# Kernel optimization log

Measured on AMD Instinct MI355X. Metric: run time of the kernel, lower is better.

The kernel has to match this reference:

```python
import jax, jax.numpy as jnp
import numpy as np

H = 8          # heads
C = 128        # out_channels per head (hidden_dim)
EMB = 256      # embedding_dim
NG = 64        # number of graphs in batch
EPS_LN = 1e-5


def _layer_norm(x, g, b):
    mu = x.mean(-1, keepdims=True)
    var = ((x - mu) ** 2).mean(-1, keepdims=True)
    return (x - mu) * jax.lax.rsqrt(var + EPS_LN) * g + b


def _transformer_conv(x, src, dst, Wq, bq, Wk, bk, Wv, bv, Ws, bs, Wb):
    # PyG TransformerConv, heads=H, concat=False, beta=True, root_weight=True
    N = x.shape[0]
    q = (x @ Wq + bq).reshape(N, H, C)
    k = (x @ Wk + bk).reshape(N, H, C)
    v = (x @ Wv + bv).reshape(N, H, C)
    # per-edge attention logits: q_i . k_j / sqrt(C)   (i=dst, j=src)
    logits = jnp.einsum('ehc,ehc->eh', q[dst], k[src]) / jnp.sqrt(jnp.asarray(C, x.dtype))
    # segment softmax over incoming edges of each dst node
    m = jax.ops.segment_max(logits, dst, num_segments=N)
    m = jnp.where(jnp.isfinite(m), m, 0.0)
    ex = jnp.exp(logits - m[dst])
    den = jax.ops.segment_sum(ex, dst, num_segments=N)
    alpha = ex / (den[dst] + 1e-16)                      # [E,H]
    msg = alpha[:, :, None] * v[src]                     # [E,H,C]
    out = jax.ops.segment_sum(msg, dst, num_segments=N)  # [N,H,C]
    out = out.mean(axis=1)                               # concat=False -> head mean
    # beta-gated skip connection
    x_r = x @ Ws + bs                                    # [N,C]
    beta = jax.nn.sigmoid(jnp.concatenate([out, x_r, out - x_r], axis=-1) @ Wb)  # [N,1]
    return beta * x_r + (1.0 - beta) * out


def _lin(k, fan_in, fan_out, scale=None):
    s = scale if scale is not None else 1.0 / np.sqrt(fan_in)
    k1, k2 = jax.random.split(k)
    W = jax.random.uniform(k1, (fan_in, fan_out), jnp.float32, -s, s)
    b = jax.random.uniform(k2, (fan_out,), jnp.float32, -s, s)
    return W, b


def setup_inputs() -> dict:
    key = jax.random.key(0)
    ks = jax.random.split(key, 32)
    N, E, V = 50000, 400000, 10000
    inp = {
        'x': jax.random.randint(ks[0], (N,), 0, V, jnp.int32),
        'edge_index': jax.random.randint(ks[1], (2, E), 0, N, jnp.int32),
        'batch': jnp.sort(jax.random.randint(ks[2], (N,), 0, NG, jnp.int32)),
        'emb_w': jax.random.normal(ks[3], (V, EMB), jnp.float32),
    }
    ki = 4
    for l, din in enumerate([EMB, C]):
        Wq, bq = _lin(ks[ki], din, H * C); ki += 1
        Wk, bk = _lin(ks[ki], din, H * C); ki += 1
        Wv, bv = _lin(ks[ki], din, H * C); ki += 1
        Ws, bs = _lin(ks[ki], din, C); ki += 1
        Wb, _ = _lin(ks[ki], 3 * C, 1); ki += 1
        inp.update({f'Wq{l}': Wq, f'bq{l}': bq, f'Wk{l}': Wk, f'bk{l}': bk,
                    f'Wv{l}': Wv, f'bv{l}': bv, f'Ws{l}': Ws, f'bs{l}': bs,
                    f'Wb{l}': Wb, f'g{l}': jnp.ones((C,), jnp.float32),
                    f'be{l}': jnp.zeros((C,), jnp.float32)})
    Wc1, bc1 = _lin(ks[ki], C, C // 2); ki += 1
    Wc2, bc2 = _lin(ks[ki], C // 2, 1); ki += 1
    inp.update({'Wc1': Wc1, 'bc1': bc1, 'Wc2': Wc2, 'bc2': bc2})
    return inp


def reference(x, edge_index, batch, emb_w,
              Wq0, bq0, Wk0, bk0, Wv0, bv0, Ws0, bs0, Wb0, g0, be0,
              Wq1, bq1, Wk1, bk1, Wv1, bv1, Ws1, bs1, Wb1, g1, be1,
              Wc1, bc1, Wc2, bc2):
    src, dst = edge_index[0], edge_index[1]
    h = emb_w[x]                                           # [N, EMB]
    # layer 0 (no residual, per original `if i > 0`)
    h = _transformer_conv(h, src, dst, Wq0, bq0, Wk0, bk0, Wv0, bv0, Ws0, bs0, Wb0)
    h = jax.nn.relu(_layer_norm(h, g0, be0))               # dropout = identity (eval)
    # layer 1 (residual)
    res = h
    h = _transformer_conv(h, src, dst, Wq1, bq1, Wk1, bk1, Wv1, bv1, Ws1, bs1, Wb1)
    h = jax.nn.relu(_layer_norm(h + res, g1, be1))
    # global mean pool over graphs
    s = jax.ops.segment_sum(h, batch, num_segments=NG)     # [NG, C]
    cnt = jax.ops.segment_sum(jnp.ones((h.shape[0],), h.dtype), batch, num_segments=NG)
    pooled = s / jnp.maximum(cnt, 1.0)[:, None]
    # classifier MLP
    z = jax.nn.relu(pooled @ Wc1 + bc1)
    return z @ Wc2 + bc2                                   # [NG, 1]
```

## Files before the change

### kernel.cpp

```cpp
#include <hip/hip_runtime.h>
#include <hip/hip_fp16.h>
#include <math.h>

#define HEADS 8
#define CDIM 128
#define HC 1024
#define EMBD 256
#define NGRAPH 64
#define QSCALE 0.08838834764831845f
#define QSCALE2 0.12751744f

typedef unsigned short u16;
typedef short s8v __attribute__((ext_vector_type(8)));
typedef float f4v __attribute__((ext_vector_type(4)));
typedef _Float16 h2v __attribute__((ext_vector_type(2)));

__device__ __forceinline__ float b2f(u16 u) {
  union { unsigned int i; float f; } v; v.i = ((unsigned int)u) << 16; return v.f;
}
__device__ __forceinline__ u16 f2b(float f) {
  union { float f; unsigned int i; } v; v.f = f;
  unsigned int i = v.i;
  unsigned int r = (i + 0x7FFFu + ((i >> 16) & 1u)) >> 16;
  return (u16)r;
}
__device__ __forceinline__ u16 f2h(float f) {
  __half h = __float2half(f);
  return *(u16*)&h;
}

union U4H { uint4 u; h2v h[4]; };

__device__ __forceinline__ float dot8h(uint4 ku, uint4 qu0, uint4 qu1) {
  (void)qu1;
  return 0.f;
}

__global__ __launch_bounds__(256) void embed_kernel(
    const int* __restrict__ x, const float* __restrict__ emb,
    u16* __restrict__ h0, int N)
{
  int idx = blockIdx.x * 256 + threadIdx.x;
  if (idx >= N * (EMBD / 4)) return;
  int n = idx >> 6;
  int j = (idx & 63) * 4;
  int vid = x[n];
  float4 f = *(const float4*)&emb[(size_t)vid * EMBD + j];
  ushort4 u;
  u.x = f2b(f.x); u.y = f2b(f.y); u.z = f2b(f.z); u.w = f2b(f.w);
  *(ushort4*)&h0[(size_t)n * EMBD + j] = u;
}

__global__ __launch_bounds__(256) void transposeWs_tiled(
    const float* __restrict__ in, u16* __restrict__ out, int R)
{
  __shared__ u16 tile[64][66];
  int r0 = blockIdx.x * 64, c0 = blockIdx.y * 64;
  int t = threadIdx.x;
  int ci = t & 63, q4 = t >> 6;
#pragma unroll
  for (int ii = 0; ii < 16; ii++) {
    int r = q4 + ii * 4;
    tile[r][ci] = f2b(in[(size_t)(r0 + r) * CDIM + c0 + ci]);
  }
  __syncthreads();
  int rr = t & 63;
#pragma unroll
  for (int ii = 0; ii < 16; ii++) {
    int c = q4 + ii * 4;
    out[(size_t)(c0 + c) * R + r0 + rr] = tile[rr][c];
  }
}

__global__ __launch_bounds__(256) void build_qkvT_tiled(
    const float* __restrict__ Wq, const float* __restrict__ Wk, const float* __restrict__ Wv,
    u16* __restrict__ WT, int K, int hpc)
{
  __shared__ u16 tile[64][130];
  int rg0 = blockIdx.x * 128;
  int kk0 = blockIdx.y * 64;
  int chunkCols = hpc * 384;
  int chunk = rg0 / chunkCols;
  int within = rg0 - chunk * chunkCols;
  int head = chunk * hpc + within / 384;
  int sub = within % 384;
  int sect = sub >> 7;
  const float* W = (sect == 0) ? Wq : (sect == 1 ? Wk : Wv);
  float scale = (sect == 0) ? QSCALE2 : 1.0f;
  int cc0 = head * CDIM;
  int t = threadIdx.x;
  int ci = t & 127, k2 = t >> 7;
#pragma unroll
  for (int ii = 0; ii < 32; ii++) {
    int ki = k2 + ii * 2;
    tile[ki][ci] = f2b(W[(size_t)(kk0 + ki) * HC + cc0 + ci] * scale);
  }
  __syncthreads();
  int k = t & 63, r4 = t >> 6;
#pragma unroll
  for (int ii = 0; ii < 32; ii++) {
    int r = r4 + ii * 4;
    WT[(size_t)(rg0 + r) * K + kk0 + k] = tile[k][r];
  }
}
__global__ __launch_bounds__(256) void build_qkvb(
    const float* __restrict__ bq, const float* __restrict__ bk, const float* __restrict__ bv,
    float* __restrict__ bT, int hpc)
{
  int rg = blockIdx.x * 256 + threadIdx.x;
  if (rg >= 3 * HC) return;
  int chunkCols = hpc * 384;
  int chunk = rg / chunkCols;
  int within = rg - chunk * chunkCols;
  int head = chunk * hpc + within / 384;
  int sub = within % 384;
  int sect = sub >> 7;
  int cc = head * CDIM + (sub & 127);
  bT[rg] = (sect == 0) ? bq[cc] * QSCALE2 : (sect == 1 ? bk[cc] : bv[cc]);
}

__global__ __launch_bounds__(256) void deg_kernel(const int* __restrict__ ei, int* __restrict__ deg, int E) {
  int e = blockIdx.x * 256 + threadIdx.x;
  if (e < E) atomicAdd(&deg[ei[E + e]], 1);
}
__global__ __launch_bounds__(256) void scan1_kernel(const int* __restrict__ deg, int* __restrict__ row_ptr,
                                                    int* __restrict__ bsum, int N) {
  __shared__ int sb[256];
  int t = threadIdx.x, idx = blockIdx.x * 256 + t;
  int x = (idx < N) ? deg[idx] : 0;
  sb[t] = x; __syncthreads();
  for (int off = 1; off < 256; off <<= 1) {
    int y = (t >= off) ? sb[t - off] : 0;
    __syncthreads(); sb[t] += y; __syncthreads();
  }
  if (idx < N) row_ptr[idx + 1] = sb[t];
  if (t == 255) bsum[blockIdx.x] = sb[255];
  if (idx == 0) row_ptr[0] = 0;
}
__global__ __launch_bounds__(256) void scan2_kernel(int* __restrict__ bsum, int B) {
  __shared__ int sb[256];
  int t = threadIdx.x;
  int x = (t < B) ? bsum[t] : 0;
  sb[t] = x; __syncthreads();
  for (int off = 1; off < 256; off <<= 1) {
    int y = (t >= off) ? sb[t - off] : 0;
    __syncthreads(); sb[t] += y; __syncthreads();
  }
  if (t < B) bsum[t] = sb[t] - x;
}
__global__ __launch_bounds__(256) void scan3_kernel(int* __restrict__ row_ptr, const int* __restrict__ bsum, int N) {
  int idx = blockIdx.x * 256 + threadIdx.x;
  if (idx < N) row_ptr[idx + 1] += bsum[idx >> 8];
}
__global__ __launch_bounds__(256) void scatter_kernel(const int* __restrict__ ei,
                                                      const int* __restrict__ row_ptr,
                                                      int* __restrict__ fill, int* __restrict__ col, int E) {
  int e = blockIdx.x * 256 + threadIdx.x;
  if (e >= E) return;
  int d = ei[E + e];
  int pos = row_ptr[d] + atomicAdd(&fill[d], 1);
  col[pos] = ei[e];
}
__global__ void gb_kernel(const int* __restrict__ batch, int* __restrict__ gb, int N) {
  int g = threadIdx.x;
  if (g > NGRAPH) return;
  int lo = 0, hi = N;
  while (lo < hi) { int mid = (lo + hi) >> 1; if (batch[mid] < g) lo = mid + 1; else hi = mid; }
  gb[g] = lo;
}

template <int K, int F16OUT>
__global__ __launch_bounds__(256, 2) void gemm_lds(
    const u16* __restrict__ A, const u16* __restrict__ BT,
    const float* __restrict__ bias, u16* __restrict__ outT,
    int M, int Ncol)
{
  const int LDK = K + 8;
  const int KS = K / 32;
  __shared__ __align__(16) u16 As[64 * LDK];
  int t = threadIdx.x, lane = t & 63, w = t >> 6;
  int q4 = lane >> 4, cn = lane & 15;
  int m0 = blockIdx.y * 64;
  int nt = blockIdx.x * 4 + w;
  bool wActive = nt * 64 < Ncol;

  if (m0 + 64 <= M) {
    const u16* Ablk = A + (size_t)m0 * K;
#pragma unroll
    for (int ii = 0; ii < K / 32; ii++) {
      int g = (ii * 256 + t) * 8;
      int r = g / K, c = g - r * K;
      *(uint4*)&As[r * LDK + c] = *(const uint4*)(Ablk + g);
    }
  } else {
#pragma unroll
    for (int ii = 0; ii < K / 32; ii++) {
      int g = (ii * 256 + t) * 8;
      int r = g / K, c = g - r * K;
      int gr = m0 + r; if (gr >= M) gr = M - 1;
      *(uint4*)&As[r * LDK + c] = *(const uint4*)(A + (size_t)gr * K + c);
    }
  }
  __syncthreads();

  if (!wActive) return;

  f4v acc[4][4] = {};
  const u16* bb = BT + ((size_t)nt * 64 + cn) * K + q4 * 8;
#pragma unroll
  for (int ks = 0; ks < KS; ks++) {
    s8v bf[4], af[4];
#pragma unroll
    for (int ni = 0; ni < 4; ni++)
      bf[ni] = *(const s8v*)(bb + (size_t)ni * 16 * K + ks * 32);
#pragma unroll
    for (int mi = 0; mi < 4; mi++)
      af[mi] = *(const s8v*)&As[(mi * 16 + cn) * LDK + ks * 32 + q4 * 8];
#pragma unroll
    for (int mi = 0; mi < 4; mi++)
#pragma unroll
      for (int ni = 0; ni < 4; ni++)
        acc[mi][ni] = __builtin_amdgcn_mfma_f32_16x16x32_bf16(af[mi], bf[ni], acc[mi][ni], 0, 0, 0);
  }

  u16* obase = outT + (size_t)nt * M * 64;
  float bv[4];
#pragma unroll
  for (int ni = 0; ni < 4; ni++) bv[ni] = bias[nt * 64 + ni * 16 + cn];
#pragma unroll
  for (int mi = 0; mi < 4; mi++) {
#pragma unroll
    for (int j = 0; j < 4; j++) {
      int gm = m0 + mi * 16 + q4 * 4 + j;
      if (gm < M) {
#pragma unroll
        for (int ni = 0; ni < 4; ni++) {
          float val = acc[mi][ni][j] + bv[ni];
          obase[(size_t)gm * 64 + ni * 16 + cn] = F16OUT ? f2h(val) : f2b(val);
        }
      }
    }
  }
}

template <int HPC>
__global__ __launch_bounds__(256) void attn_chunk_kernel(
    const u16* __restrict__ qkv,
    const int* __restrict__ row_ptr, const int* __restrict__ col,
    float* __restrict__ outacc, int N, int first)
{
  int t = threadIdx.x;
  int w = t >> 6, lane = t & 63;
  int g = lane >> 4, i = lane & 15;
  int n, j;
  if (HPC == 4)      { n = blockIdx.x;                 j = w; }
  else if (HPC == 2) { n = blockIdx.x * 2 + (w >> 1);  j = w & 1; }
  else               { n = blockIdx.x * 4 + w;         j = 0; }
  bool active = (HPC == 4) ? true : (n < N);

  int itile = i >> 3, ioff = (i & 7) * 8;
  const u16* qb = qkv + (size_t)(j * 6 + 0 + itile) * N * 64 + ioff;
  const u16* kb = qkv + (size_t)(j * 6 + 2 + itile) * N * 64 + ioff;
  const u16* vb = qkv + (size_t)(j * 6 + 4 + itile) * N * 64 + ioff;

  float acc[8] = {};
  float m = -INFINITY, l = 0.f;
  if (active) {
    U4H qu; qu.u = *(const uint4*)(qb + (size_t)n * 64);
    int e0 = row_ptr[n], e1 = row_ptr[n + 1];
    for (int eb = e0; eb < e1; eb += 8) {
      int egA = eb + g, egB = eb + 4 + g;
      bool vA = egA < e1, vB = egB < e1;
      int sA = col[vA ? egA : e1 - 1];
      int sB = col[vB ? egB : e1 - 1];
      U4H kuA, vuA, kuB, vuB;
      kuA.u = *(const uint4*)(kb + (size_t)sA * 64);
      kuB.u = *(const uint4*)(kb + (size_t)sB * 64);
      vuA.u = *(const uint4*)(vb + (size_t)sA * 64);
      vuB.u = *(const uint4*)(vb + (size_t)sB * 64);

      float pA, pB;
#if defined(__has_builtin) && __has_builtin(__builtin_amdgcn_fdot2)
      pA = __builtin_amdgcn_fdot2(kuA.h[0], qu.h[0], 0.f, false);
      pA = __builtin_amdgcn_fdot2(kuA.h[1], qu.h[1], pA, false);
      pA = __builtin_amdgcn_fdot2(kuA.h[2], qu.h[2], pA, false);
      pA = __builtin_amdgcn_fdot2(kuA.h[3], qu.h[3], pA, false);
      pB = __builtin_amdgcn_fdot2(kuB.h[0], qu.h[0], 0.f, false);
      pB = __builtin_amdgcn_fdot2(kuB.h[1], qu.h[1], pB, false);
      pB = __builtin_amdgcn_fdot2(kuB.h[2], qu.h[2], pB, false);
      pB = __builtin_amdgcn_fdot2(kuB.h[3], qu.h[3], pB, false);
#else
      pA = 0.f; pB = 0.f;
#pragma unroll
      for (int z = 0; z < 4; z++) {
        pA += (float)kuA.h[z][0] * (float)qu.h[z][0] + (float)kuA.h[z][1] * (float)qu.h[z][1];
        pB += (float)kuB.h[z][0] * (float)qu.h[z][0] + (float)kuB.h[z][1] * (float)qu.h[z][1];
      }
#endif
#pragma unroll
      for (int off = 1; off <= 8; off <<= 1) {
        pA += __shfl_xor(pA, off, 64);
        pB += __shfl_xor(pB, off, 64);
      }
      if (!vA) pA = -INFINITY;
      if (!vB) pB = -INFINITY;

      {
        float pm = fmaxf(pA, __shfl_xor(pA, 16));
        pm = fmaxf(pm, __shfl_xor(pm, 32));
        if (pm > m) {
          float al = exp2f(m - pm);
          l *= al;
#pragma unroll
          for (int z = 0; z < 8; z++) acc[z] *= al;
          m = pm;
        }
        float pe = exp2f(pA - m);
        float ps = pe + __shfl_xor(pe, 16);
        ps += __shfl_xor(ps, 32);
        l += ps;
#pragma unroll
        for (int z = 0; z < 4; z++) {
          acc[2 * z]     = fmaf(pe, (float)vuA.h[z][0], acc[2 * z]);
          acc[2 * z + 1] = fmaf(pe, (float)vuA.h[z][1], acc[2 * z + 1]);
        }
      }
      {
        float pm = fmaxf(pB, __shfl_xor(pB, 16));
        pm = fmaxf(pm, __shfl_xor(pm, 32));
        if (pm > m) {
          float al = exp2f(m - pm);
          l *= al;
#pragma unroll
          for (int z = 0; z < 8; z++) acc[z] *= al;
          m = pm;
        }
        float pe = exp2f(pB - m);
        float ps = pe + __shfl_xor(pe, 16);
        ps += __shfl_xor(ps, 32);
        l += ps;
#pragma unroll
        for (int z = 0; z < 4; z++) {
          acc[2 * z]     = fmaf(pe, (float)vuB.h[z][0], acc[2 * z]);
          acc[2 * z + 1] = fmaf(pe, (float)vuB.h[z][1], acc[2 * z + 1]);
        }
      }
    }
  }
  float inv = 0.125f / (l + 1e-16f);
#pragma unroll
  for (int z = 0; z < 8; z++) {
    float a = acc[z] * inv;
    a += __shfl_xor(a, 16);
    a += __shfl_xor(a, 32);
    acc[z] = a;
  }

  if (HPC == 1) {
    if (active && g == 0) {
      float* op = outacc + (size_t)n * CDIM + i * 8;
      if (first) {
        *(float4*)op       = make_float4(acc[0], acc[1], acc[2], acc[3]);
        *(float4*)(op + 4) = make_float4(acc[4], acc[5], acc[6], acc[7]);
      } else {
        float4 o0 = *(float4*)op, o1 = *(float4*)(op + 4);
        *(float4*)op       = make_float4(o0.x + acc[0], o0.y + acc[1], o0.z + acc[2], o0.w + acc[3]);
        *(float4*)(op + 4) = make_float4(o1.x + acc[4], o1.y + acc[5], o1.z + acc[6], o1.w + acc[7]);
      }
    }
  } else {
    __shared__ float sacc[4][128];
    if (g == 0) {
      *(float4*)&sacc[w][i * 8]     = make_float4(acc[0], acc[1], acc[2], acc[3]);
      *(float4*)&sacc[w][i * 8 + 4] = make_float4(acc[4], acc[5], acc[6], acc[7]);
    }
    __syncthreads();
    if (HPC == 4) {
      if (t < 128) {
        float v = sacc[0][t] + sacc[1][t] + sacc[2][t] + sacc[3][t];
        size_t o = (size_t)blockIdx.x * CDIM + t;
        outacc[o] = first ? v : (outacc[o] + v);
      }
    } else {
      int nn = blockIdx.x * 2 + (t >> 7);
      int c = t & 127;
      if (nn < N) {
        float v = sacc[(t >> 7) * 2][c] + sacc[(t >> 7) * 2 + 1][c];
        size_t o = (size_t)nn * CDIM + c;
        outacc[o] = first ? v : (outacc[o] + v);
      }
    }
  }
}

template <int LAYER>
__global__ __launch_bounds__(256) void epilogue_kernel(
    const float* __restrict__ outacc, const u16* __restrict__ xrT,
    const float* __restrict__ Wb, const float* __restrict__ gam, const float* __restrict__ bet,
    const u16* __restrict__ res,
    u16* __restrict__ hout,
    float* __restrict__ houtf,
    int N)
{
  int t = threadIdx.x;
  int local = t >> 7, c = t & 127, w = t >> 6;
  int n = blockIdx.x * 2 + local;
  bool act = n < N;
  __shared__ float sred[8];
  __shared__ float smv[2][3];

  float oc = 0.f, xc = 0.f;
  if (act) {
    oc = outacc[(size_t)n * CDIM + c];
    xc = b2f(xrT[((size_t)(c >> 6) * N + n) * 64 + (c & 63)]);
  }
  float pb = oc * Wb[c] + xc * Wb[CDIM + c] + (oc - xc) * Wb[2 * CDIM + c];
#pragma unroll
  for (int off = 32; off; off >>= 1) pb += __shfl_down(pb, off, 64);
  if ((t & 63) == 0) sred[w] = pb;
  __syncthreads();
  if (t == 0)   smv[0][0] = 1.f / (1.f + __expf(-(sred[0] + sred[1])));
  if (t == 128) smv[1][0] = 1.f / (1.f + __expf(-(sred[2] + sred[3])));
  __syncthreads();
  float beta = smv[local][0];
  float val = beta * xc + (1.f - beta) * oc;
  if (LAYER == 1 && act) val += b2f(res[(size_t)n * CDIM + c]);

  float s1 = val, s2 = val * val;
#pragma unroll
  for (int off = 32; off; off >>= 1) {
    s1 += __shfl_down(s1, off, 64);
    s2 += __shfl_down(s2, off, 64);
  }
  __syncthreads();
  if ((t & 63) == 0) { sred[w * 2] = s1; sred[w * 2 + 1] = s2; }
  __syncthreads();
  if (t == 0) {
    float S1 = sred[0] + sred[2], S2 = sred[1] + sred[3];
    float mu = S1 * (1.f / CDIM);
    float var = fmaxf(S2 * (1.f / CDIM) - mu * mu, 0.f);
    smv[0][1] = mu; smv[0][2] = 1.f / sqrtf(var + 1e-5f);
  }
  if (t == 128) {
    float S1 = sred[4] + sred[6], S2 = sred[5] + sred[7];
    float mu = S1 * (1.f / CDIM);
    float var = fmaxf(S2 * (1.f / CDIM) - mu * mu, 0.f);
    smv[1][1] = mu; smv[1][2] = 1.f / sqrtf(var + 1e-5f);
  }
  __syncthreads();
  if (act) {
    float y = (val - smv[local][1]) * smv[local][2] * gam[c] + bet[c];
    y = fmaxf(y, 0.f);
    if (LAYER == 0) hout[(size_t)n * CDIM + c] = f2b(y);
    else            houtf[(size_t)n * CDIM + c] = y;
  }
}

__global__ __launch_bounds__(256) void classifier_kernel(
    const float* __restrict__ hf, const int* __restrict__ gb,
    const float* __restrict__ Wc1, const float* __restrict__ bc1,
    const float* __restrict__ Wc2, const float* __restrict__ bc2,
    float* __restrict__ out)
{
  int g = blockIdx.x, t = threadIdx.x;
  int half = t >> 7, c = t & 127;
  int s = gb[g], e = gb[g + 1];
  float acc = 0.f;
  for (int n = s + half; n < e; n += 2) acc += hf[(size_t)n * CDIM + c];
  __shared__ float sb[2][128];
  __shared__ float sp[128], sz[64];
  sb[half][c] = acc;
  __syncthreads();
  float cg = fmaxf((float)(e - s), 1.f);
  if (t < 128) sp[t] = (sb[0][t] + sb[1][t]) / cg;
  __syncthreads();
  if (t < 64) {
    float a = bc1[t];
    for (int cc = 0; cc < 128; cc++) a += sp[cc] * Wc1[cc * 64 + t];
    sz[t] = fmaxf(a, 0.f);
  }
  __syncthreads();
  if (t < 64) {
    float pbv = sz[t] * Wc2[t];
    for (int off = 32; off; off >>= 1) pbv += __shfl_down(pbv, off, 64);
    if (t == 0) out[g] = pbv + bc2[0];
  }
}

extern "C" void kernel_launch(void* const* d_in, const int* in_sizes, int n_in,
                              void* d_out, int out_size, void* d_ws, size_t ws_size,
                              hipStream_t stream)
{
  if (n_in != 30) return;

  const int N = in_sizes[0];
  const int E = in_sizes[1] / 2;

  const int* x     = (const int*)d_in[0];
  const int* ei    = (const int*)d_in[1];
  const int* batch = (const int*)d_in[2];
  const float* emb = (const float*)d_in[3];
  const float* Wq0 = (const float*)d_in[4];  const float* bq0 = (const float*)d_in[5];
  const float* Wk0 = (const float*)d_in[6];  const float* bk0 = (const float*)d_in[7];
  const float* Wv0 = (const float*)d_in[8];  const float* bv0 = (const float*)d_in[9];
  const float* Ws0 = (const float*)d_in[10]; const float* bs0 = (const float*)d_in[11];
  const float* Wb0 = (const float*)d_in[12]; const float* g0  = (const float*)d_in[13]; const float* be0 = (const float*)d_in[14];
  const float* Wq1 = (const float*)d_in[15]; const float* bq1 = (const float*)d_in[16];
  const float* Wk1 = (const float*)d_in[17]; const float* bk1 = (const float*)d_in[18];
  const float* Wv1 = (const float*)d_in[19]; const float* bv1 = (const float*)d_in[20];
  const float* Ws1 = (const float*)d_in[21]; const float* bs1 = (const float*)d_in[22];
  const float* Wb1 = (const float*)d_in[23]; const float* g1  = (const float*)d_in[24]; const float* be1 = (const float*)d_in[25];
  const float* Wc1 = (const float*)d_in[26]; const float* bc1 = (const float*)d_in[27];
  const float* Wc2 = (const float*)d_in[28]; const float* bc2 = (const float*)d_in[29];

  auto rnd = [](size_t b) { return (b + 511) & ~(size_t)511; };
  size_t fixedBytes =
      rnd((size_t)N * CDIM * 4) +
      rnd((size_t)N * EMBD * 2) +
      rnd((size_t)N * CDIM * 2) * 2 +
      rnd((size_t)3 * HC * EMBD * 2) +
      rnd((size_t)3 * HC * CDIM * 2) +
      rnd((size_t)3 * HC * 4) * 2 +
      rnd((size_t)CDIM * EMBD * 2) +
      rnd((size_t)CDIM * CDIM * 2) +
      rnd((size_t)N * 4) * 2 +
      rnd((size_t)(N + 1) * 4) +
      rnd((size_t)E * 4) +
      rnd(256 * 4) +
      rnd(65 * 4);
  int hpc = 1;
  if (ws_size >= fixedBytes + rnd((size_t)N * 4 * 384 * 2)) hpc = 4;
  else if (ws_size >= fixedBytes + rnd((size_t)N * 2 * 384 * 2)) hpc = 2;
  const int chunkCols = hpc * 384;
  const int nchunks = HEADS / hpc;

  char* ws = (char*)d_ws;
  size_t off = 0;
  auto alloc = [&](size_t bytes) -> void* {
    void* p = ws + off;
    off += (bytes + 511) & ~(size_t)511;
    return p;
  };
  u16*   qkvc  = (u16*)  alloc((size_t)N * chunkCols * 2);
  float* outacc= (float*)alloc((size_t)N * CDIM * 4);
  u16*   h0    = (u16*)  alloc((size_t)N * EMBD * 2);
  u16*   h1    = (u16*)  alloc((size_t)N * CDIM * 2);
  u16*   xrb   = (u16*)  alloc((size_t)N * CDIM * 2);
  u16*   WT0   = (u16*)  alloc((size_t)3 * HC * EMBD * 2);
  u16*   WT1   = (u16*)  alloc((size_t)3 * HC * CDIM * 2);
  float* bT0   = (float*)alloc((size_t)3 * HC * 4);
  float* bT1   = (float*)alloc((size_t)3 * HC * 4);
  u16*   WsT0  = (u16*)  alloc((size_t)CDIM * EMBD * 2);
  u16*   WsT1  = (u16*)  alloc((size_t)CDIM * CDIM * 2);
  int*   deg   = (int*)  alloc((size_t)N * 4);
  int*   fill  = (int*)  alloc((size_t)N * 4);
  int*   rowp  = (int*)  alloc((size_t)(N + 1) * 4);
  int*   colb  = (int*)  alloc((size_t)E * 4);
  int*   bsum  = (int*)  alloc(256 * 4);
  int*   gb    = (int*)  alloc(65 * 4);

  hipMemsetAsync(deg, 0, (size_t)N * 4, stream);
  hipMemsetAsync(fill, 0, (size_t)N * 4, stream);

  embed_kernel<<<(N * 64 + 255) / 256, 256, 0, stream>>>(x, emb, h0, N);
  { dim3 gT(3 * HC / 128, EMBD / 64);
    build_qkvT_tiled<<<gT, 256, 0, stream>>>(Wq0, Wk0, Wv0, WT0, EMBD, hpc); }
  { dim3 gT(3 * HC / 128, CDIM / 64);
    build_qkvT_tiled<<<gT, 256, 0, stream>>>(Wq1, Wk1, Wv1, WT1, CDIM, hpc); }
  build_qkvb<<<(3 * HC + 255) / 256, 256, 0, stream>>>(bq0, bk0, bv0, bT0, hpc);
  build_qkvb<<<(3 * HC + 255) / 256, 256, 0, stream>>>(bq1, bk1, bv1, bT1, hpc);
  { dim3 gT(EMBD / 64, CDIM / 64);
    transposeWs_tiled<<<gT, 256, 0, stream>>>(Ws0, WsT0, EMBD); }
  { dim3 gT(CDIM / 64, CDIM / 64);
    transposeWs_tiled<<<gT, 256, 0, stream>>>(Ws1, WsT1, CDIM); }

  int nb = (N + 255) / 256;
  deg_kernel<<<(E + 255) / 256, 256, 0, stream>>>(ei, deg, E);
  scan1_kernel<<<nb, 256, 0, stream>>>(deg, rowp, bsum, N);
  scan2_kernel<<<1, 256, 0, stream>>>(bsum, nb);
  scan3_kernel<<<nb, 256, 0, stream>>>(rowp, bsum, N);
  scatter_kernel<<<(E + 255) / 256, 256, 0, stream>>>(ei, rowp, fill, colb, E);
  gb_kernel<<<1, 128, 0, stream>>>(batch, gb, N);

  int rowStrips = (N + 63) / 64;
  int attnBlocks = (hpc == 4) ? N : (hpc == 2 ? (N + 1) / 2 : (N + 3) / 4);
  int epiBlocks = (N + 1) / 2;

  for (int layer = 0; layer < 2; layer++) {
    const u16* Ain   = (layer == 0) ? h0 : h1;
    const u16* WT    = (layer == 0) ? WT0 : WT1;
    const float* bT  = (layer == 0) ? bT0 : bT1;
    const u16* WsT   = (layer == 0) ? WsT0 : WsT1;
    const float* bs  = (layer == 0) ? bs0 : bs1;
    const float* Wb  = (layer == 0) ? Wb0 : Wb1;
    const float* gam = (layer == 0) ? g0 : g1;
    const float* bet = (layer == 0) ? be0 : be1;
    int K = (layer == 0) ? EMBD : CDIM;

    dim3 gXR(1, rowStrips);
    dim3 gQKV(chunkCols / 256, rowStrips);
    if (K == EMBD) gemm_lds<EMBD, 0><<<gXR, 256, 0, stream>>>(Ain, WsT, bs, xrb, N, CDIM);
    else           gemm_lds<CDIM, 0><<<gXR, 256, 0, stream>>>(Ain, WsT, bs, xrb, N, CDIM);
    for (int c = 0; c < nchunks; c++) {
      if (K == EMBD)
        gemm_lds<EMBD, 1><<<gQKV, 256, 0, stream>>>(Ain, WT + (size_t)c * chunkCols * K,
                                                    bT + c * chunkCols, qkvc, N, chunkCols);
      else
        gemm_lds<CDIM, 1><<<gQKV, 256, 0, stream>>>(Ain, WT + (size_t)c * chunkCols * K,
                                                    bT + c * chunkCols, qkvc, N, chunkCols);
      int first = (c == 0) ? 1 : 0;
      if (hpc == 4)      attn_chunk_kernel<4><<<attnBlocks, 256, 0, stream>>>(qkvc, rowp, colb, outacc, N, first);
      else if (hpc == 2) attn_chunk_kernel<2><<<attnBlocks, 256, 0, stream>>>(qkvc, rowp, colb, outacc, N, first);
      else               attn_chunk_kernel<1><<<attnBlocks, 256, 0, stream>>>(qkvc, rowp, colb, outacc, N, first);
    }
    if (layer == 0) {
      epilogue_kernel<0><<<epiBlocks, 256, 0, stream>>>(outacc, xrb, Wb, gam, bet,
                                                        (const u16*)nullptr, h1, (float*)nullptr, N);
    } else {
      epilogue_kernel<1><<<epiBlocks, 256, 0, stream>>>(outacc, xrb, Wb, gam, bet,
                                                        h1, (u16*)nullptr, (float*)qkvc, N);
    }
  }

  classifier_kernel<<<NGRAPH, 256, 0, stream>>>((const float*)qkvc, gb, Wc1, bc1, Wc2, bc2,
                                                (float*)d_out);
}
```

Baseline: 1.251 ms.

## Pre-swizzle GEMM weights into MFMA fragment order and widen attention edge parallelism

Weight matrices are now written in a layout that matches the MFMA B-fragment order, so each lane loads its 16-byte fragment contiguously instead of strided rows of the transposed weight. The attention kernel switches from 4-edges-by-16-lanes to 8-edges-by-8-lanes, so each lane handles 16 channels and a wave processes 8 edges per online-softmax step with a single rescale. GEMM occupancy hint is raised to 3 blocks per SM. The changes aim to cut B-operand load inefficiency and per-edge shuffle/rescale overhead, at the cost of more registers per lane in attention.

Result: no change. 1.255 ms (+0.3%).

```diff
diff --git a/kernel.cpp b/kernel.cpp
--- a/kernel.cpp
+++ b/kernel.cpp
@@ -30,11 +30,6 @@
 }
 
 union U4H { uint4 u; h2v h[4]; };
-
-__device__ __forceinline__ float dot8h(uint4 ku, uint4 qu0, uint4 qu1) {
-  (void)qu1;
-  return 0.f;
-}
 
 __global__ __launch_bounds__(256) void embed_kernel(
     const int* __restrict__ x, const float* __restrict__ emb,
@@ -51,32 +46,30 @@
   *(ushort4*)&h0[(size_t)n * EMBD + j] = u;
 }
 
-__global__ __launch_bounds__(256) void transposeWs_tiled(
-    const float* __restrict__ in, u16* __restrict__ out, int R)
-{
-  __shared__ u16 tile[64][66];
-  int r0 = blockIdx.x * 64, c0 = blockIdx.y * 64;
+__global__ __launch_bounds__(256) void build_WsT_swz(
+    const float* __restrict__ in, u16* __restrict__ out, int K)
+{
+  const int KS = K / 32;
+  int nt = blockIdx.x;
+  int ks = blockIdx.y;
   int t = threadIdx.x;
-  int ci = t & 63, q4 = t >> 6;
-#pragma unroll
-  for (int ii = 0; ii < 16; ii++) {
-    int r = q4 + ii * 4;
-    tile[r][ci] = f2b(in[(size_t)(r0 + r) * CDIM + c0 + ci]);
-  }
-  __syncthreads();
-  int rr = t & 63;
-#pragma unroll
-  for (int ii = 0; ii < 16; ii++) {
-    int c = q4 + ii * 4;
-    out[(size_t)(c0 + c) * R + r0 + rr] = tile[rr][c];
-  }
-}
-
-__global__ __launch_bounds__(256) void build_qkvT_tiled(
+  int lane = t & 63, ni = t >> 6;
+  int q4 = lane >> 4, cn = lane & 15;
+  int colL = nt * 64 + ni * 16 + cn;
+  int kbase = ks * 32 + q4 * 8;
+  u16 tmp[8];
+#pragma unroll
+  for (int e8 = 0; e8 < 8; e8++) tmp[e8] = f2b(in[(size_t)(kbase + e8) * CDIM + colL]);
+  size_t base = ((((size_t)nt * KS + ks) * 4 + ni) * 64 + lane) * 8;
+  *(uint4*)&out[base] = *(uint4*)tmp;
+}
+
+__global__ __launch_bounds__(256) void build_qkvT_swz(
     const float* __restrict__ Wq, const float* __restrict__ Wk, const float* __restrict__ Wv,
     u16* __restrict__ WT, int K, int hpc)
 {
   __shared__ u16 tile[64][130];
+  const int KS = K / 32;
   int rg0 = blockIdx.x * 128;
   int kk0 = blockIdx.y * 64;
   int chunkCols = hpc * 384;
@@ -96,11 +89,23 @@
     tile[ki][ci] = f2b(W[(size_t)(kk0 + ki) * HC + cc0 + ci] * scale);
   }
   __syncthreads();
-  int k = t & 63, r4 = t >> 6;
-#pragma unroll
-  for (int ii = 0; ii < 32; ii++) {
-    int r = r4 + ii * 4;
-    WT[(size_t)(rg0 + r) * K + kk0 + k] = tile[k][r];
+
+  int lane = t & 63, ni = t >> 6;
+  int q4 = lane >> 4, cn = lane & 15;
+  int ntBase = rg0 >> 6;
+#pragma unroll
+  for (int ntd = 0; ntd < 2; ntd++) {
+#pragma unroll
+    for (int ksd = 0; ksd < 2; ksd++) {
+      if (ksd * 32 >= 64) continue;
+      int colL = ntd * 64 + ni * 16 + cn;
+      int kL = ksd * 32 + q4 * 8;
+      u16 tmp[8];
+#pragma unroll
+      for (int e8 = 0; e8 < 8; e8++) tmp[e8] = tile[kL + e8][colL];
+      size_t base = ((((size_t)(ntBase + ntd) * KS + (kk0 >> 5) + ksd) * 4 + ni) * 64 + lane) * 8;
+      *(uint4*)&WT[base] = *(uint4*)tmp;
+    }
   }
 }
 __global__ __launch_bounds__(256) void build_qkvb(
@@ -170,8 +175,8 @@
 }
 
 template <int K, int F16OUT>
-__global__ __launch_bounds__(256, 2) void gemm_lds(
-    const u16* __restrict__ A, const u16* __restrict__ BT,
+__global__ __launch_bounds__(256, 3) void gemm_lds(
+    const u16* __restrict__ A, const u16* __restrict__ Bswz, int col0tile,
     const float* __restrict__ bias, u16* __restrict__ outT,
     int M, int Ncol)
 {
@@ -181,8 +186,9 @@
   int t = threadIdx.x, lane = t & 63, w = t >> 6;
   int q4 = lane >> 4, cn = lane & 15;
   int m0 = blockIdx.y * 64;
-  int nt = blockIdx.x * 4 + w;
-  bool wActive = nt * 64 < Ncol;
+  int ntL = blockIdx.x * 4 + w;
+  bool wActive = ntL * 64 < Ncol;
+  int ntG = col0tile + ntL;
 
   if (m0 + 64 <= M) {
     const u16* Ablk = A + (size_t)m0 * K;
@@ -206,13 +212,13 @@
   if (!wActive) return;
 
   f4v acc[4][4] = {};
-  const u16* bb = BT + ((size_t)nt * 64 + cn) * K + q4 * 8;
+  const u16* bb = Bswz + ((size_t)ntG * KS * 4) * 64 * 8 + lane * 8;
 #pragma unroll
   for (int ks = 0; ks < KS; ks++) {
     s8v bf[4], af[4];
 #pragma unroll
     for (int ni = 0; ni < 4; ni++)
-      bf[ni] = *(const s8v*)(bb + (size_t)ni * 16 * K + ks * 32);
+      bf[ni] = *(const s8v*)(bb + ((size_t)ks * 4 + ni) * 64 * 8);
 #pragma unroll
     for (int mi = 0; mi < 4; mi++)
       af[mi] = *(const s8v*)&As[(mi * 16 + cn) * LDK + ks * 32 + q4 * 8];
@@ -223,10 +229,10 @@
         acc[mi][ni] = __builtin_amdgcn_mfma_f32_16x16x32_bf16(af[mi], bf[ni], acc[mi][ni], 0, 0, 0);
   }
 
-  u16* obase = outT + (size_t)nt * M * 64;
+  u16* obase = outT + (size_t)ntL * M * 64;
   float bv[4];
 #pragma unroll
-  for (int ni = 0; ni < 4; ni++) bv[ni] = bias[nt * 64 + ni * 16 + cn];
+  for (int ni = 0; ni < 4; ni++) bv[ni] = bias[ntG * 64 + ni * 16 + cn];
 #pragma unroll
   for (int mi = 0; mi < 4; mi++) {
 #pragma unroll
@@ -251,128 +257,114 @@
 {
   int t = threadIdx.x;
   int w = t >> 6, lane = t & 63;
-  int g = lane >> 4, i = lane & 15;
+  int e = lane >> 3, i = lane & 7;
   int n, j;
   if (HPC == 4)      { n = blockIdx.x;                 j = w; }
   else if (HPC == 2) { n = blockIdx.x * 2 + (w >> 1);  j = w & 1; }
   else               { n = blockIdx.x * 4 + w;         j = 0; }
   bool active = (HPC == 4) ? true : (n < N);
 
-  int itile = i >> 3, ioff = (i & 7) * 8;
+  int itile = i >> 2, ioff = (i & 3) * 16;
   const u16* qb = qkv + (size_t)(j * 6 + 0 + itile) * N * 64 + ioff;
   const u16* kb = qkv + (size_t)(j * 6 + 2 + itile) * N * 64 + ioff;
   const u16* vb = qkv + (size_t)(j * 6 + 4 + itile) * N * 64 + ioff;
 
-  float acc[8] = {};
+  float acc[16] = {};
   float m = -INFINITY, l = 0.f;
   if (active) {
-    U4H qu; qu.u = *(const uint4*)(qb + (size_t)n * 64);
+    U4H qu0, qu1;
+    qu0.u = *(const uint4*)(qb + (size_t)n * 64);
+    qu1.u = *(const uint4*)(qb + (size_t)n * 64 + 8);
     int e0 = row_ptr[n], e1 = row_ptr[n + 1];
     for (int eb = e0; eb < e1; eb += 8) {
-      int egA = eb + g, egB = eb + 4 + g;
-      bool vA = egA < e1, vB = egB < e1;
-      int sA = col[vA ? egA : e1 - 1];
-      int sB = col[vB ? egB : e1 - 1];
-      U4H kuA, vuA, kuB, vuB;
-      kuA.u = *(const uint4*)(kb + (size_t)sA * 64);
-      kuB.u = *(const uint4*)(kb + (size_t)sB * 64);
-      vuA.u = *(const uint4*)(vb + (size_t)sA * 64);
-      vuB.u = *(const uint4*)(vb + (size_t)sB * 64);
-
-      float pA, pB;
+      int eg = eb + e;
+      bool val = eg < e1;
+      int s = col[val ? eg : e1 - 1];
+      const u16* kp = kb + (size_t)s * 64;
+      const u16* vp = vb + (size_t)s * 64;
+      U4H ku0, ku1, vu0, vu1;
+      ku0.u = *(const uint4*)kp;
+      ku1.u = *(const uint4*)(kp + 8);
+      vu0.u = *(const uint4*)vp;
+      vu1.u = *(const uint4*)(vp + 8);
+
+      float p;
 #if defined(__has_builtin) && __has_builtin(__builtin_amdgcn_fdot2)
-      pA = __builtin_amdgcn_fdot2(kuA.h[0], qu.h[0], 0.f, false);
-      pA = __builtin_amdgcn_fdot2(kuA.h[1], qu.h[1], pA, false);
-      pA = __builtin_amdgcn_fdot2(kuA.h[2], qu.h[2], pA, false);
-      pA = __builtin_amdgcn_fdot2(kuA.h[3], qu.h[3], pA, false);
-      pB = __builtin_amdgcn_fdot2(kuB.h[0], qu.h[0], 0.f, false);
-      pB = __builtin_amdgcn_fdot2(kuB.h[1], qu.h[1], pB, false);
-      pB = __builtin_amdgcn_fdot2(kuB.h[2], qu.h[2], pB, false);
-      pB = __builtin_amdgcn_fdot2(kuB.h[3], qu.h[3], pB, false);
+      p = __builtin_amdgcn_fdot2(ku0.h[0], qu0.h[0], 0.f, false);
+      p = __builtin_amdgcn_fdot2(ku0.h[1], qu0.h[1], p, false);
+      p = __builtin_amdgcn_fdot2(ku0.h[2], qu0.h[2], p, false);
+      p = __builtin_amdgcn_fdot2(ku0.h[3], qu0.h[3], p, false);
+      p = __builtin_amdgcn_fdot2(ku1.h[0], qu1.h[0], p, false);
+      p = __builtin_amdgcn_fdot2(ku1.h[1], qu1.h[1], p, false);
+      p = __builtin_amdgcn_fdot2(ku1.h[2], qu1.h[2], p, false);
+      p = __builtin_amdgcn_fdot2(ku1.h[3], qu1.h[3], p, false);
 #else
-      pA = 0.f; pB = 0.f;
+      p = 0.f;
 #pragma unroll
       for (int z = 0; z < 4; z++) {
-        pA += (float)kuA.h[z][0] * (float)qu.h[z][0] + (float)kuA.h[z][1] * (float)qu.h[z][1];
-        pB += (float)kuB.h[z][0] * (float)qu.h[z][0] + (float)kuB.h[z][1] * (float)qu.h[z][1];
+        p += (float)ku0.h[z][0] * (float)qu0.h[z][0] + (float)ku0.h[z][1] * (float)qu0.h[z][1];
+        p += (float)ku1.h[z][0] * (float)qu1.h[z][0] + (float)ku1.h[z][1] * (float)qu1.h[z][1];
       }
 #endif
-#pragma unroll
-      for (int off = 1; off <= 8; off <<= 1) {
-        pA += __shfl_xor(pA, off, 64);
-        pB += __shfl_xor(pB, off, 64);
+      p += __shfl_xor(p, 1); p += __shfl_xor(p, 2); p += __shfl_xor(p, 4);
+      if (!val) p = -INFINITY;
+      float pm = fmaxf(p, __shfl_xor(p, 8));
+      pm = fmaxf(pm, __shfl_xor(pm, 16));
+      pm = fmaxf(pm, __shfl_xor(pm, 32));
+      if (pm > m) {
+        float al = exp2f(m - pm);
+        l *= al;
+#pragma unroll
+        for (int z = 0; z < 16; z++) acc[z] *= al;
+        m = pm;
       }
-      if (!vA) pA = -INFINITY;
-      if (!vB) pB = -INFINITY;
-
-      {
-        float pm = fmaxf(pA, __shfl_xor(pA, 16));
-        pm = fmaxf(pm, __shfl_xor(pm, 32));
-        if (pm > m) {
-          float al = exp2f(m - pm);
-          l *= al;
-#pragma unroll
-          for (int z = 0; z < 8; z++) acc[z] *= al;
-          m = pm;
-        }
-        float pe = exp2f(pA - m);
-        float ps = pe + __shfl_xor(pe, 16);
-        ps += __shfl_xor(ps, 32);
-        l += ps;
-#pragma unroll
-        for (int z = 0; z < 4; z++) {
-          acc[2 * z]     = fmaf(pe, (float)vuA.h[z][0], acc[2 * z]);
-          acc[2 * z + 1] = fmaf(pe, (float)vuA.h[z][1], acc[2 * z + 1]);
-        }
+      float pe = exp2f(p - m);
+      float ps = pe + __shfl_xor(pe, 8);
+      ps += __shfl_xor(ps, 16);
+      ps += __shfl_xor(ps, 32);
+      l += ps;
+#pragma unroll
+      for (int z = 0; z < 4; z++) {
+        acc[2 * z]     = fmaf(pe, (float)vu0.h[z][0], acc[2 * z]);
+        acc[2 * z + 1] = fmaf(pe, (float)vu0.h[z][1], acc[2 * z + 1]);
+        acc[8 + 2 * z]     = fmaf(pe, (float)vu1.h[z][0], acc[8 + 2 * z]);
+        acc[8 + 2 * z + 1] = fmaf(pe, (float)vu1.h[z][1], acc[8 + 2 * z + 1]);
       }
-      {
-        float pm = fmaxf(pB, __shfl_xor(pB, 16));
-        pm = fmaxf(pm, __shfl_xor(pm, 32));
-        if (pm > m) {
-          float al = exp2f(m - pm);
-          l *= al;
-#pragma unroll
-          for (int z = 0; z < 8; z++) acc[z] *= al;
-          m = pm;
-        }
-        float pe = exp2f(pB - m);
-        float ps = pe + __shfl_xor(pe, 16);
-        ps += __shfl_xor(ps, 32);
-        l += ps;
-#pragma unroll
-        for (int z = 0; z < 4; z++) {
-          acc[2 * z]     = fmaf(pe, (float)vuB.h[z][0], acc[2 * z]);
-          acc[2 * z + 1] = fmaf(pe, (float)vuB.h[z][1], acc[2 * z + 1]);
-        }
-      }
     }
   }
   float inv = 0.125f / (l + 1e-16f);
 #pragma unroll
-  for (int z = 0; z < 8; z++) {
+  for (int z = 0; z < 16; z++) {
     float a = acc[z] * inv;
+    a += __shfl_xor(a, 8);
     a += __shfl_xor(a, 16);
     a += __shfl_xor(a, 32);
     acc[z] = a;
   }
 
   if (HPC == 1) {
-    if (active && g == 0) {
-      float* op = outacc + (size_t)n * CDIM + i * 8;
+    if (active && e == 0) {
+      float* op = outacc + (size_t)n * CDIM + i * 16;
       if (first) {
-        *(float4*)op       = make_float4(acc[0], acc[1], acc[2], acc[3]);
-        *(float4*)(op + 4) = make_float4(acc[4], acc[5], acc[6], acc[7]);
+#pragma unroll
+        for (int z4 = 0; z4 < 4; z4++)
+          *(float4*)(op + z4 * 4) = make_float4(acc[z4*4], acc[z4*4+1], acc[z4*4+2], acc[z4*4+3]);
       } else {
-        float4 o0 = *(float4*)op, o1 = *(float4*)(op + 4);
-        *(float4*)op       = make_float4(o0.x + acc[0], o0.y + acc[1], o0.z + acc[2], o0.w + acc[3]);
-        *(float4*)(op + 4) = make_float4(o1.x + acc[4], o1.y + acc[5], o1.z + acc[6], o1.w + acc[7]);
+#pragma unroll
+        for (int z4 = 0; z4 < 4; z4++) {
+          float4 o = *(float4*)(op + z4 * 4);
+          *(float4*)(op + z4 * 4) = make_float4(o.x + acc[z4*4], o.y + acc[z4*4+1],
+                                                o.z + acc[z4*4+2], o.w + acc[z4*4+3]);
+        }
       }
     }
   } else {
     __shared__ float sacc[4][128];
-    if (g == 0) {
-      *(float4*)&sacc[w][i * 8]     = make_float4(acc[0], acc[1], acc[2], acc[3]);
-      *(float4*)&sacc[w][i * 8 + 4] = make_float4(acc[4], acc[5], acc[6], acc[7]);
+    if (e == 0) {
+#pragma unroll
+      for (int z4 = 0; z4 < 4; z4++)
+        *(float4*)&sacc[w][i * 16 + z4 * 4] =
+            make_float4(acc[z4*4], acc[z4*4+1], acc[z4*4+2], acc[z4*4+3]);
     }
     __syncthreads();
     if (HPC == 4) {
@@ -564,15 +556,15 @@
 
   embed_kernel<<<(N * 64 + 255) / 256, 256, 0, stream>>>(x, emb, h0, N);
   { dim3 gT(3 * HC / 128, EMBD / 64);
-    build_qkvT_tiled<<<gT, 256, 0, stream>>>(Wq0, Wk0, Wv0, WT0, EMBD, hpc); }
+    build_qkvT_swz<<<gT, 256, 0, stream>>>(Wq0, Wk0, Wv0, WT0, EMBD, hpc); }
   { dim3 gT(3 * HC / 128, CDIM / 64);
-    build_qkvT_tiled<<<gT, 256, 0, stream>>>(Wq1, Wk1, Wv1, WT1, CDIM, hpc); }
+    build_qkvT_swz<<<gT, 256, 0, stream>>>(Wq1, Wk1, Wv1, WT1, CDIM, hpc); }
   build_qkvb<<<(3 * HC + 255) / 256, 256, 0, stream>>>(bq0, bk0, bv0, bT0, hpc);
   build_qkvb<<<(3 * HC + 255) / 256, 256, 0, stream>>>(bq1, bk1, bv1, bT1, hpc);
-  { dim3 gT(EMBD / 64, CDIM / 64);
-    transposeWs_tiled<<<gT, 256, 0, stream>>>(Ws0, WsT0, EMBD); }
-  { dim3 gT(CDIM / 64, CDIM / 64);
-    transposeWs_tiled<<<gT, 256, 0, stream>>>(Ws1, WsT1, CDIM); }
+  { dim3 gT(2, EMBD / 32);
+    build_WsT_swz<<<gT, 256, 0, stream>>>(Ws0, WsT0, EMBD); }
+  { dim3 gT(2, CDIM / 32);
+    build_WsT_swz<<<gT, 256, 0, stream>>>(Ws1, WsT1, CDIM); }
 
   int nb = (N + 255) / 256;
   deg_kernel<<<(E + 255) / 256, 256, 0, stream>>>(ei, deg, E);
@@ -598,16 +590,15 @@
     int K = (layer == 0) ? EMBD : CDIM;
 
     dim3 gXR(1, rowStrips);
-    dim3 gQKV(chunkCols / 256, rowStrips);
-    if (K == EMBD) gemm_lds<EMBD, 0><<<gXR, 256, 0, stream>>>(Ain, WsT, bs, xrb, N, CDIM);
-    else           gemm_lds<CDIM, 0><<<gXR, 256, 0, stream>>>(Ain, WsT, bs, xrb, N, CDIM);
+    dim3 gQKV((chunkCols + 255) / 256, rowStrips);
+    if (K == EMBD) gemm_lds<EMBD, 0><<<gXR, 256, 0, stream>>>(Ain, WsT, 0, bs, xrb, N, CDIM);
+    else           gemm_lds<CDIM, 0><<<gXR, 256, 0, stream>>>(Ain, WsT, 0, bs, xrb, N, CDIM);
     for (int c = 0; c < nchunks; c++) {
+      int col0tile = c * (chunkCols / 64);
       if (K == EMBD)
-        gemm_lds<EMBD, 1><<<gQKV, 256, 0, stream>>>(Ain, WT + (size_t)c * chunkCols * K,
-                                                    bT + c * chunkCols, qkvc, N, chunkCols);
+        gemm_lds<EMBD, 1><<<gQKV, 256, 0, stream>>>(Ain, WT, col0tile, bT, qkvc, N, chunkCols);
       else
-        gemm_lds<CDIM, 1><<<gQKV, 256, 0, stream>>>(Ain, WT + (size_t)c * chunkCols * K,
-                                                    bT + c * chunkCols, qkvc, N, chunkCols);
+        gemm_lds<CDIM, 1><<<gQKV, 256, 0, stream>>>(Ain, WT, col0tile, bT, qkvc, N, chunkCols);
       int first = (c == 0) ? 1 : 0;
       if (hpc == 4)      attn_chunk_kernel<4><<<attnBlocks, 256, 0, stream>>>(qkvc, rowp, colb, outacc, N, first);
       else if (hpc == 2) attn_chunk_kernel<2><<<attnBlocks, 256, 0, stream>>>(qkvc, rowp, colb, outacc, N, first);
```

## Pre-swizzle GEMM B weights into MFMA fragment order for coalesced loads

Applied to the files above, without the earlier changes.

Weight transpose kernels now write the Q/K/V and skip-projection weights in a swizzled layout that matches the per-lane MFMA B-fragment order. Each wave's B loads then read contiguous 16-byte chunks across lanes instead of strided rows. The GEMM takes a column tile offset rather than pointer arithmetic, the grid rounds up, and launch bounds are raised to allow three blocks per CU. The risk is register spilling from the tighter occupancy target, and the gain depends on how bound the GEMMs are by B reads, since B is mostly cache-resident.

Result: faster. 1.137 ms (-9.1%).

```diff
diff --git a/kernel.cpp b/kernel.cpp
--- a/kernel.cpp
+++ b/kernel.cpp
@@ -30,11 +30,6 @@
 }
 
 union U4H { uint4 u; h2v h[4]; };
-
-__device__ __forceinline__ float dot8h(uint4 ku, uint4 qu0, uint4 qu1) {
-  (void)qu1;
-  return 0.f;
-}
 
 __global__ __launch_bounds__(256) void embed_kernel(
     const int* __restrict__ x, const float* __restrict__ emb,
@@ -51,32 +46,30 @@
   *(ushort4*)&h0[(size_t)n * EMBD + j] = u;
 }
 
-__global__ __launch_bounds__(256) void transposeWs_tiled(
-    const float* __restrict__ in, u16* __restrict__ out, int R)
-{
-  __shared__ u16 tile[64][66];
-  int r0 = blockIdx.x * 64, c0 = blockIdx.y * 64;
+__global__ __launch_bounds__(256) void build_WsT_swz(
+    const float* __restrict__ in, u16* __restrict__ out, int K)
+{
+  const int KS = K / 32;
+  int nt = blockIdx.x;
+  int ks = blockIdx.y;
   int t = threadIdx.x;
-  int ci = t & 63, q4 = t >> 6;
-#pragma unroll
-  for (int ii = 0; ii < 16; ii++) {
-    int r = q4 + ii * 4;
-    tile[r][ci] = f2b(in[(size_t)(r0 + r) * CDIM + c0 + ci]);
-  }
-  __syncthreads();
-  int rr = t & 63;
-#pragma unroll
-  for (int ii = 0; ii < 16; ii++) {
-    int c = q4 + ii * 4;
-    out[(size_t)(c0 + c) * R + r0 + rr] = tile[rr][c];
-  }
-}
-
-__global__ __launch_bounds__(256) void build_qkvT_tiled(
+  int lane = t & 63, ni = t >> 6;
+  int q4 = lane >> 4, cn = lane & 15;
+  int colL = nt * 64 + ni * 16 + cn;
+  int kbase = ks * 32 + q4 * 8;
+  u16 tmp[8];
+#pragma unroll
+  for (int e8 = 0; e8 < 8; e8++) tmp[e8] = f2b(in[(size_t)(kbase + e8) * CDIM + colL]);
+  size_t base = ((((size_t)nt * KS + ks) * 4 + ni) * 64 + lane) * 8;
+  *(uint4*)&out[base] = *(uint4*)tmp;
+}
+
+__global__ __launch_bounds__(256) void build_qkvT_swz(
     const float* __restrict__ Wq, const float* __restrict__ Wk, const float* __restrict__ Wv,
     u16* __restrict__ WT, int K, int hpc)
 {
   __shared__ u16 tile[64][130];
+  const int KS = K / 32;
   int rg0 = blockIdx.x * 128;
   int kk0 = blockIdx.y * 64;
   int chunkCols = hpc * 384;
@@ -96,11 +89,22 @@
     tile[ki][ci] = f2b(W[(size_t)(kk0 + ki) * HC + cc0 + ci] * scale);
   }
   __syncthreads();
-  int k = t & 63, r4 = t >> 6;
-#pragma unroll
-  for (int ii = 0; ii < 32; ii++) {
-    int r = r4 + ii * 4;
-    WT[(size_t)(rg0 + r) * K + kk0 + k] = tile[k][r];
+
+  int lane = t & 63, ni = t >> 6;
+  int q4 = lane >> 4, cn = lane & 15;
+  int ntBase = rg0 >> 6;
+#pragma unroll
+  for (int ntd = 0; ntd < 2; ntd++) {
+#pragma unroll
+    for (int ksd = 0; ksd < 2; ksd++) {
+      int colL = ntd * 64 + ni * 16 + cn;
+      int kL = ksd * 32 + q4 * 8;
+      u16 tmp[8];
+#pragma unroll
+      for (int e8 = 0; e8 < 8; e8++) tmp[e8] = tile[kL + e8][colL];
+      size_t base = ((((size_t)(ntBase + ntd) * KS + (kk0 >> 5) + ksd) * 4 + ni) * 64 + lane) * 8;
+      *(uint4*)&WT[base] = *(uint4*)tmp;
+    }
   }
 }
 __global__ __launch_bounds__(256) void build_qkvb(
@@ -170,8 +174,8 @@
 }
 
 template <int K, int F16OUT>
-__global__ __launch_bounds__(256, 2) void gemm_lds(
-    const u16* __restrict__ A, const u16* __restrict__ BT,
+__global__ __launch_bounds__(256, 3) void gemm_lds(
+    const u16* __restrict__ A, const u16* __restrict__ Bswz, int col0tile,
     const float* __restrict__ bias, u16* __restrict__ outT,
     int M, int Ncol)
 {
@@ -181,8 +185,9 @@
   int t = threadIdx.x, lane = t & 63, w = t >> 6;
   int q4 = lane >> 4, cn = lane & 15;
   int m0 = blockIdx.y * 64;
-  int nt = blockIdx.x * 4 + w;
-  bool wActive = nt * 64 < Ncol;
+  int ntL = blockIdx.x * 4 + w;
+  bool wActive = ntL * 64 < Ncol;
+  int ntG = col0tile + ntL;
 
   if (m0 + 64 <= M) {
     const u16* Ablk = A + (size_t)m0 * K;
@@ -206,13 +211,13 @@
   if (!wActive) return;
 
   f4v acc[4][4] = {};
-  const u16* bb = BT + ((size_t)nt * 64 + cn) * K + q4 * 8;
+  const u16* bb = Bswz + ((size_t)ntG * KS * 4) * 64 * 8 + lane * 8;
 #pragma unroll
   for (int ks = 0; ks < KS; ks++) {
     s8v bf[4], af[4];
 #pragma unroll
     for (int ni = 0; ni < 4; ni++)
-      bf[ni] = *(const s8v*)(bb + (size_t)ni * 16 * K + ks * 32);
+      bf[ni] = *(const s8v*)(bb + ((size_t)ks * 4 + ni) * 64 * 8);
 #pragma unroll
     for (int mi = 0; mi < 4; mi++)
       af[mi] = *(const s8v*)&As[(mi * 16 + cn) * LDK + ks * 32 + q4 * 8];
@@ -223,10 +228,10 @@
         acc[mi][ni] = __builtin_amdgcn_mfma_f32_16x16x32_bf16(af[mi], bf[ni], acc[mi][ni], 0, 0, 0);
   }
 
-  u16* obase = outT + (size_t)nt * M * 64;
+  u16* obase = outT + (size_t)ntL * M * 64;
   float bv[4];
 #pragma unroll
-  for (int ni = 0; ni < 4; ni++) bv[ni] = bias[nt * 64 + ni * 16 + cn];
+  for (int ni = 0; ni < 4; ni++) bv[ni] = bias[ntG * 64 + ni * 16 + cn];
 #pragma unroll
   for (int mi = 0; mi < 4; mi++) {
 #pragma unroll
@@ -564,15 +569,15 @@
 
   embed_kernel<<<(N * 64 + 255) / 256, 256, 0, stream>>>(x, emb, h0, N);
   { dim3 gT(3 * HC / 128, EMBD / 64);
-    build_qkvT_tiled<<<gT, 256, 0, stream>>>(Wq0, Wk0, Wv0, WT0, EMBD, hpc); }
+    build_qkvT_swz<<<gT, 256, 0, stream>>>(Wq0, Wk0, Wv0, WT0, EMBD, hpc); }
   { dim3 gT(3 * HC / 128, CDIM / 64);
-    build_qkvT_tiled<<<gT, 256, 0, stream>>>(Wq1, Wk1, Wv1, WT1, CDIM, hpc); }
+    build_qkvT_swz<<<gT, 256, 0, stream>>>(Wq1, Wk1, Wv1, WT1, CDIM, hpc); }
   build_qkvb<<<(3 * HC + 255) / 256, 256, 0, stream>>>(bq0, bk0, bv0, bT0, hpc);
   build_qkvb<<<(3 * HC + 255) / 256, 256, 0, stream>>>(bq1, bk1, bv1, bT1, hpc);
-  { dim3 gT(EMBD / 64, CDIM / 64);
-    transposeWs_tiled<<<gT, 256, 0, stream>>>(Ws0, WsT0, EMBD); }
-  { dim3 gT(CDIM / 64, CDIM / 64);
-    transposeWs_tiled<<<gT, 256, 0, stream>>>(Ws1, WsT1, CDIM); }
+  { dim3 gT(2, EMBD / 32);
+    build_WsT_swz<<<gT, 256, 0, stream>>>(Ws0, WsT0, EMBD); }
+  { dim3 gT(2, CDIM / 32);
+    build_WsT_swz<<<gT, 256, 0, stream>>>(Ws1, WsT1, CDIM); }
 
   int nb = (N + 255) / 256;
   deg_kernel<<<(E + 255) / 256, 256, 0, stream>>>(ei, deg, E);
@@ -598,16 +603,15 @@
     int K = (layer == 0) ? EMBD : CDIM;
 
     dim3 gXR(1, rowStrips);
-    dim3 gQKV(chunkCols / 256, rowStrips);
-    if (K == EMBD) gemm_lds<EMBD, 0><<<gXR, 256, 0, stream>>>(Ain, WsT, bs, xrb, N, CDIM);
-    else           gemm_lds<CDIM, 0><<<gXR, 256, 0, stream>>>(Ain, WsT, bs, xrb, N, CDIM);
+    dim3 gQKV((chunkCols + 255) / 256, rowStrips);
+    if (K == EMBD) gemm_lds<EMBD, 0><<<gXR, 256, 0, stream>>>(Ain, WsT, 0, bs, xrb, N, CDIM);
+    else           gemm_lds<CDIM, 0><<<gXR, 256, 0, stream>>>(Ain, WsT, 0, bs, xrb, N, CDIM);
     for (int c = 0; c < nchunks; c++) {
+      int col0tile = c * (chunkCols / 64);
       if (K == EMBD)
-        gemm_lds<EMBD, 1><<<gQKV, 256, 0, stream>>>(Ain, WT + (size_t)c * chunkCols * K,
-                                                    bT + c * chunkCols, qkvc, N, chunkCols);
+        gemm_lds<EMBD, 1><<<gQKV, 256, 0, stream>>>(Ain, WT, col0tile, bT, qkvc, N, chunkCols);
       else
-        gemm_lds<CDIM, 1><<<gQKV, 256, 0, stream>>>(Ain, WT + (size_t)c * chunkCols * K,
-                                                    bT + c * chunkCols, qkvc, N, chunkCols);
+        gemm_lds<CDIM, 1><<<gQKV, 256, 0, stream>>>(Ain, WT, col0tile, bT, qkvc, N, chunkCols);
       int first = (c == 0) ? 1 : 0;
       if (hpc == 4)      attn_chunk_kernel<4><<<attnBlocks, 256, 0, stream>>>(qkvc, rowp, colb, outacc, N, first);
       else if (hpc == 2) attn_chunk_kernel<2><<<attnBlocks, 256, 0, stream>>>(qkvc, rowp, colb, outacc, N, first);
```
